# Optimization experiments

Measured on AMD Instinct MI355X. Metric: run time of the kernel, lower is better.

The kernel has to match this reference:

```python
import jax, jax.numpy as jnp
import numpy as np

B, S, D_MODEL = 4, 2048, 1024
H, DK, DV = 16, 64, 64
MASKED = False


def setup_inputs() -> dict:
    key = jax.random.key(0)
    ks = jax.random.split(key, 7)
    return {
        "q": jax.random.normal(ks[0], (B, S, D_MODEL), dtype=jnp.float32),
        "k": jax.random.normal(ks[1], (B, S, D_MODEL), dtype=jnp.float32),
        "v": jax.random.normal(ks[2], (B, S, D_MODEL), dtype=jnp.float32),
        "Wq": jax.random.normal(ks[3], (H, D_MODEL, DK), dtype=jnp.float32) * 0.05,
        "Wk": jax.random.normal(ks[4], (H, D_MODEL, DK), dtype=jnp.float32) * 0.05,
        "Wv": jax.random.normal(ks[5], (H, D_MODEL, DV), dtype=jnp.float32) * 0.05,
        "Wo": jax.random.normal(ks[6], (H * DV, D_MODEL), dtype=jnp.float32) * 0.05,
    }


def reference(q, k, v, Wq, Wk, Wv, Wo):
    # Per-head projections, batched over heads instead of a Python loop.
    Q = jnp.einsum("bsd,hdk->bhsk", q, Wq)  # [B,H,S,Dk]
    K = jnp.einsum("btd,hdk->bhtk", k, Wk)  # [B,H,S,Dk]
    V = jnp.einsum("btd,hdv->bhtv", v, Wv)  # [B,H,S,Dv]

    scale = 1.0 / jnp.sqrt(jnp.asarray(DK, dtype=Q.dtype))
    scores = jnp.einsum("bhsk,bhtk->bhst", Q, K) * scale  # [B,H,S,S]
    if MASKED:
        causal = jnp.tril(jnp.ones((S, S), dtype=bool))
        scores = jnp.where(causal, scores, jnp.finfo(scores.dtype).min)
    attn = jax.nn.softmax(scores, axis=-1)
    heads = jnp.einsum("bhst,bhtv->bhsv", attn, V)  # [B,H,S,Dv]

    # concat heads along feature dim (tf.concat(heads, axis=-1)) then Wo projection
    multi = heads.transpose(0, 2, 1, 3).reshape(q.shape[0], q.shape[1], H * DV)
    return multi @ Wo  # [B,S,D_MODEL]
```

## Files before the change

### kernel.cpp

```cpp
#include <hip/hip_runtime.h>
#include <hip/hip_bf16.h>

typedef __attribute__((ext_vector_type(8))) short short8;
typedef __attribute__((ext_vector_type(4))) short short4v;
typedef __attribute__((ext_vector_type(4))) float f32x4;
typedef __attribute__((ext_vector_type(2))) float f32x2;
typedef __attribute__((ext_vector_type(4))) unsigned short us4;
typedef __attribute__((ext_vector_type(2))) unsigned int u32x2;

#define NB 4
#define SEQ 2048
#define DMODEL 1024
#define NH 16
#define DHEAD 64
#define QSCALE 0.18033688011112042f
#define FM 34.0f

static __device__ __forceinline__ unsigned short f2bf(float f) {
    __hip_bfloat16 h = __float2bfloat16(f);
    return *reinterpret_cast<unsigned short*>(&h);
}
static __device__ __forceinline__ unsigned int cvt_pk(float lo, float hi) {
    float2 t; t.x = lo; t.y = hi;
    __hip_bfloat162 h = __float22bfloat162_rn(t);
    return *reinterpret_cast<unsigned int*>(&h);
}

typedef __attribute__((address_space(3))) unsigned int lds_u32_t;
typedef __attribute__((address_space(1))) const unsigned int glob_u32_t;
static __device__ __forceinline__ void gl_lds16(const unsigned short* g, unsigned short* l) {
    __builtin_amdgcn_global_load_lds((glob_u32_t*)g, (lds_u32_t*)l, 16, 0, 0);
}

__global__ __launch_bounds__(256) void prep_all(const float* __restrict__ q,
                                                const float* __restrict__ k,
                                                const float* __restrict__ v,
                                                const float* __restrict__ wq,
                                                const float* __restrict__ wk,
                                                const float* __restrict__ wv,
                                                const float* __restrict__ wo,
                                                unsigned short* __restrict__ xq,
                                                unsigned short* __restrict__ xk,
                                                unsigned short* __restrict__ xv,
                                                unsigned short* __restrict__ oq,
                                                unsigned short* __restrict__ ok,
                                                unsigned short* __restrict__ ov,
                                                unsigned short* __restrict__ oo) {
    const int z = blockIdx.y;
    int i = blockIdx.x * 256 + threadIdx.x;
    if (z < 3) {
        const float* in = z == 0 ? q : (z == 1 ? k : v);
        unsigned short* out = z == 0 ? xq : (z == 1 ? xk : xv);
        f32x4 val = ((const f32x4*)in)[i];
        u32x2 o;
        o.x = cvt_pk(val.x, val.y);
        o.y = cvt_pk(val.z, val.w);
        ((u32x2*)out)[i] = o;
    } else {
        if (i >= NH * DMODEL * DHEAD) return;
        if (z < 6) {
            const float* w = z == 3 ? wq : (z == 4 ? wk : wv);
            unsigned short* out = z == 3 ? oq : (z == 4 ? ok : ov);
            float scale = z == 3 ? QSCALE : 1.0f;
            int kk = i & 63;
            int d  = (i >> 6) & 1023;
            int h  = i >> 16;
            out[(size_t)(h * 64 + kk) * DMODEL + d] = f2bf(w[i] * scale);
        } else {
            int c = i & 1023;
            int r = i >> 10;
            oo[(size_t)c * 1024 + r] = f2bf(wo[i]);
        }
    }
}

struct GemmAcc { f32x4 a[4][4]; };

static __device__ __forceinline__ void gemm_core(const unsigned short* __restrict__ A,
                                                 const unsigned short* __restrict__ Bt,
                                                 unsigned short (*As)[4096],
                                                 unsigned short (*Bs)[4096],
                                                 int m0, int n0, int K, GemmAcc& acc) {
    const int tid = threadIdx.x;
    const int w = tid >> 6, l = tid & 63;
    const int lane16 = l & 15, quad = l >> 4;
    const int wr = w >> 1, wc = w & 1;

#pragma unroll
    for (int a = 0; a < 4; a++)
#pragma unroll
        for (int b = 0; b < 4; b++) acc.a[a][b] = (f32x4){0.f, 0.f, 0.f, 0.f};

    const int i0 = 2 * w, i1 = 2 * w + 1;
    const int rs = l >> 2;
    const int cc = ((l & 3) ^ ((l >> 3) & 3)) * 8;
    const unsigned short* a0 = A + (size_t)(m0 + i0 * 16 + rs) * K + cc;
    const unsigned short* a1 = A + (size_t)(m0 + i1 * 16 + rs) * K + cc;
    const unsigned short* b0 = Bt + (size_t)(n0 + i0 * 16 + rs) * K + cc;
    const unsigned short* b1 = Bt + (size_t)(n0 + i1 * 16 + rs) * K + cc;

    const int cl = (quad ^ ((lane16 >> 1) & 3)) * 8;
    const int ra = (wr * 64 + lane16) * 32 + cl;
    const int rb = (wc * 64 + lane16) * 32 + cl;

    for (int k0 = 0; k0 < K; k0 += 64) {
        __syncthreads();
#pragma unroll
        for (int h = 0; h < 2; h++) {
            gl_lds16(a0 + k0 + h * 32, &As[h][i0 * 512]);
            gl_lds16(a1 + k0 + h * 32, &As[h][i1 * 512]);
            gl_lds16(b0 + k0 + h * 32, &Bs[h][i0 * 512]);
            gl_lds16(b1 + k0 + h * 32, &Bs[h][i1 * 512]);
        }
        __syncthreads();
#pragma unroll
        for (int h = 0; h < 2; h++) {
            short8 af[4], bf[4];
#pragma unroll
            for (int mt = 0; mt < 4; mt++) af[mt] = *(const short8*)&As[h][ra + mt * 512];
#pragma unroll
            for (int nt = 0; nt < 4; nt++) bf[nt] = *(const short8*)&Bs[h][rb + nt * 512];
#pragma unroll
            for (int mt = 0; mt < 4; mt++)
#pragma unroll
                for (int nt = 0; nt < 4; nt++)
                    acc.a[mt][nt] = __builtin_amdgcn_mfma_f32_16x16x32_bf16(
                        af[mt], bf[nt], acc.a[mt][nt], 0, 0, 0);
        }
    }
}

__global__ __launch_bounds__(256) void gemm_qkv(const unsigned short* __restrict__ xq,
                                                const unsigned short* __restrict__ xk,
                                                const unsigned short* __restrict__ xv,
                                                const unsigned short* __restrict__ wq,
                                                const unsigned short* __restrict__ wk,
                                                const unsigned short* __restrict__ wv,
                                                unsigned short* __restrict__ Qb,
                                                unsigned short* __restrict__ Kb,
                                                unsigned short* __restrict__ Vtb) {
    __shared__ unsigned short As[2][4096];
    __shared__ unsigned short Bs[2][4096];
    const int z = blockIdx.z;
    const unsigned short* A = z == 0 ? xq : (z == 1 ? xk : xv);
    const unsigned short* Bt = z == 0 ? wq : (z == 1 ? wk : wv);
    unsigned short* out = z == 0 ? Qb : (z == 1 ? Kb : Vtb);

    const int m0 = blockIdx.x * 128, n0 = blockIdx.y * 128;
    GemmAcc acc;
    gemm_core(A, Bt, As, Bs, m0, n0, DMODEL, acc);

    const int l = threadIdx.x & 63, w = threadIdx.x >> 6;
    const int lane16 = l & 15, quad = l >> 4;
    const int wr = w >> 1, wc = w & 1;
    if (z < 2) {
#pragma unroll
        for (int mt = 0; mt < 4; mt++)
#pragma unroll
            for (int nt = 0; nt < 4; nt++)
#pragma unroll
                for (int r = 0; r < 4; r++) {
                    int m = m0 + wr * 64 + mt * 16 + quad * 4 + r;
                    int n = n0 + wc * 64 + nt * 16 + lane16;
                    int b_ = m >> 11, s = m & 2047, h = n >> 6, kk = n & 63;
                    out[((size_t)((b_ * NH + h) * SEQ + s) << 6) + kk] = f2bf(acc.a[mt][nt][r]);
                }
    } else {
#pragma unroll
        for (int mt = 0; mt < 4; mt++)
#pragma unroll
            for (int nt = 0; nt < 4; nt++) {
                int m = m0 + wr * 64 + mt * 16 + quad * 4;
                int n = n0 + wc * 64 + nt * 16 + lane16;
                int b_ = m >> 11, s = m & 2047, h = n >> 6, kk = n & 63;
                u32x2 pk;
                pk.x = cvt_pk(acc.a[mt][nt][0], acc.a[mt][nt][1]);
                pk.y = cvt_pk(acc.a[mt][nt][2], acc.a[mt][nt][3]);
                *(u32x2*)&out[(size_t)((b_ * NH + h) * DHEAD + kk) * SEQ + s] = pk;
            }
    }
}

__global__ __launch_bounds__(256) void gemm_out(const unsigned short* __restrict__ A,
                                                const unsigned short* __restrict__ Bt,
                                                float* __restrict__ C) {
    __shared__ unsigned short As[2][4096];
    __shared__ unsigned short Bs[2][4096];
    const int m0 = blockIdx.x * 128, n0 = blockIdx.y * 128;
    GemmAcc acc;
    gemm_core(A, Bt, As, Bs, m0, n0, DMODEL, acc);

    const int l = threadIdx.x & 63, w = threadIdx.x >> 6;
    const int lane16 = l & 15, quad = l >> 4;
    const int wr = w >> 1, wc = w & 1;
#pragma unroll
    for (int mt = 0; mt < 4; mt++)
#pragma unroll
        for (int nt = 0; nt < 4; nt++)
#pragma unroll
            for (int r = 0; r < 4; r++) {
                int m = m0 + wr * 64 + mt * 16 + quad * 4 + r;
                int n = n0 + wc * 64 + nt * 16 + lane16;
                C[(size_t)m * DMODEL + n] = acc.a[mt][nt][r];
            }
}

__global__ __launch_bounds__(256) void flash_attn(const unsigned short* __restrict__ Q,
                                                  const unsigned short* __restrict__ Kg,
                                                  const unsigned short* __restrict__ Vt,
                                                  unsigned short* __restrict__ Hout) {
    __shared__ unsigned short Ks[64 * 64];
    __shared__ unsigned short Vs[64 * 64];

    const int tid = threadIdx.x;
    const int w = tid >> 6, l = tid & 63;
    const int lane16 = l & 15, quad = l >> 4;
    const int bh = blockIdx.x & 63, b_ = bh >> 4, h = bh & 15;
    const int s0 = (blockIdx.x >> 6) * 128;

    const unsigned short* Qbh = Q + (size_t)bh * SEQ * DHEAD;
    const unsigned short* Kbh = Kg + (size_t)bh * SEQ * DHEAD;
    const unsigned short* Vbh = Vt + (size_t)bh * DHEAD * SEQ;

    short8 qf[2][2];
#pragma unroll
    for (int qm = 0; qm < 2; qm++)
#pragma unroll
        for (int ks = 0; ks < 2; ks++)
            qf[qm][ks] = *(const short8*)(Qbh +
                (size_t)(s0 + w * 32 + qm * 16 + lane16) * DHEAD + ks * 32 + quad * 8);

    f32x4 o[2][4];
#pragma unroll
    for (int qm = 0; qm < 2; qm++)
#pragma unroll
        for (int dt = 0; dt < 4; dt++) o[qm][dt] = (f32x4){0.f, 0.f, 0.f, 0.f};
    f32x2 lsum2[2];
    lsum2[0] = (f32x2){0.f, 0.f};
    lsum2[1] = (f32x2){0.f, 0.f};
    const f32x4 scinit = (f32x4){-FM, -FM, -FM, -FM};

    const int i0 = 2 * w, i1 = 2 * w + 1;
    const int rs = l >> 3;
    const int cgs = ((l & 7) ^ rs) * 8;
    const unsigned short* kg0 = Kbh + (size_t)(i0 * 8 + rs) * DHEAD + cgs;
    const unsigned short* kg1 = Kbh + (size_t)(i1 * 8 + rs) * DHEAD + cgs;
    const unsigned short* vg0 = Vbh + (size_t)(i0 * 8 + rs) * SEQ + cgs;
    const unsigned short* vg1 = Vbh + (size_t)(i1 * 8 + rs) * SEQ + cgs;
    unsigned short* lk0 = &Ks[i0 * 512];
    unsigned short* lk1 = &Ks[i1 * 512];
    unsigned short* lv0 = &Vs[i0 * 512];
    unsigned short* lv1 = &Vs[i1 * 512];

    const int swz = lane16 & 7;

    for (int t0 = 0; t0 < SEQ; t0 += 64) {
        __syncthreads();
        gl_lds16(kg0 + (size_t)t0 * DHEAD, lk0);
        gl_lds16(kg1 + (size_t)t0 * DHEAD, lk1);
        gl_lds16(vg0 + t0, lv0);
        gl_lds16(vg1 + t0, lv1);
        __syncthreads();

        short4v pf[2][4];
#pragma unroll
        for (int nt = 0; nt < 4; nt++) {
            const int kbase = (nt * 16 + lane16) * 64;
            short8 kf0 = *(const short8*)&Ks[kbase + ((quad ^ swz) * 8)];
            short8 kf1 = *(const short8*)&Ks[kbase + (((4 + quad) ^ swz) * 8)];
#pragma unroll
            for (int qm = 0; qm < 2; qm++) {
                f32x4 sc = __builtin_amdgcn_mfma_f32_16x16x32_bf16(kf0, qf[qm][0], scinit, 0, 0, 0);
                sc = __builtin_amdgcn_mfma_f32_16x16x32_bf16(kf1, qf[qm][1], sc, 0, 0, 0);
                float p0 = __builtin_amdgcn_exp2f(sc.x);
                float p1 = __builtin_amdgcn_exp2f(sc.y);
                float p2 = __builtin_amdgcn_exp2f(sc.z);
                float p3 = __builtin_amdgcn_exp2f(sc.w);
                f32x2 pa; pa.x = p0; pa.y = p1;
                f32x2 pb; pb.x = p2; pb.y = p3;
                lsum2[qm] += pa;
                lsum2[qm] += pb;
                u32x2 pk;
                pk.x = cvt_pk(p0, p1);
                pk.y = cvt_pk(p2, p3);
                pf[qm][nt] = __builtin_bit_cast(short4v, pk);
            }
        }
#pragma unroll
        for (int nt = 0; nt < 4; nt++) {
#pragma unroll
            for (int dt = 0; dt < 4; dt++) {
                int cl = (2 * nt + (quad >> 1)) ^ swz;
                short4v vf = *(const short4v*)&Vs[(dt * 16 + lane16) * 64 + cl * 8 + (quad & 1) * 4];
                o[0][dt] = __builtin_amdgcn_mfma_f32_16x16x16bf16_1k(vf, pf[0][nt], o[0][dt], 0, 0, 0);
                o[1][dt] = __builtin_amdgcn_mfma_f32_16x16x16bf16_1k(vf, pf[1][nt], o[1][dt], 0, 0, 0);
            }
        }
    }

    float lsum[2];
#pragma unroll
    for (int qm = 0; qm < 2; qm++) {
        float s = lsum2[qm].x + lsum2[qm].y;
        s += __shfl_xor(s, 16);
        s += __shfl_xor(s, 32);
        lsum[qm] = s;
    }
#pragma unroll
    for (int qm = 0; qm < 2; qm++) {
        float inv = 1.f / lsum[qm];
        int s = s0 + w * 32 + qm * 16 + lane16;
        size_t rowbase = (size_t)(b_ * SEQ + s) * DMODEL + h * 64;
#pragma unroll
        for (int dt = 0; dt < 4; dt++) {
            u32x2 ov;
            ov.x = cvt_pk(o[qm][dt][0] * inv, o[qm][dt][1] * inv);
            ov.y = cvt_pk(o[qm][dt][2] * inv, o[qm][dt][3] * inv);
            *(u32x2*)&Hout[rowbase + dt * 16 + quad * 4] = ov;
        }
    }
}

extern "C" void kernel_launch(void* const* d_in, const int* in_sizes, int n_in,
                              void* d_out, int out_size, void* d_ws, size_t ws_size,
                              hipStream_t stream) {
    const float* q  = (const float*)d_in[0];
    const float* k  = (const float*)d_in[1];
    const float* v  = (const float*)d_in[2];
    const float* Wq = (const float*)d_in[3];
    const float* Wk = (const float*)d_in[4];
    const float* Wv = (const float*)d_in[5];
    const float* Wo = (const float*)d_in[6];

    const size_t SZ_X = (size_t)NB * SEQ * DMODEL * 2;
    const size_t SZ_W = (size_t)DMODEL * DMODEL * 2;
    char* ws = (char*)d_ws;
    unsigned short* xq  = (unsigned short*)(ws);
    unsigned short* xk  = (unsigned short*)(ws + SZ_X);
    unsigned short* xv  = (unsigned short*)(ws + 2 * SZ_X);
    unsigned short* wqt = (unsigned short*)(ws + 3 * SZ_X);
    unsigned short* wkt = (unsigned short*)(ws + 3 * SZ_X + SZ_W);
    unsigned short* wvt = (unsigned short*)(ws + 3 * SZ_X + 2 * SZ_W);
    unsigned short* wot = (unsigned short*)(ws + 3 * SZ_X + 3 * SZ_W);
    unsigned short* Qb  = (unsigned short*)(ws + 3 * SZ_X + 4 * SZ_W);
    unsigned short* Kb  = (unsigned short*)(ws + 4 * SZ_X + 4 * SZ_W);
    unsigned short* Vtb = (unsigned short*)(ws + 5 * SZ_X + 4 * SZ_W);
    unsigned short* hd  = (unsigned short*)(ws + 6 * SZ_X + 4 * SZ_W);
    if (ws_size < 7 * SZ_X + 4 * SZ_W) return;

    const int n4 = NB * SEQ * DMODEL / 4;
    prep_all<<<dim3(n4 / 256, 7), 256, 0, stream>>>(q, k, v, Wq, Wk, Wv, Wo,
                                                    xq, xk, xv, wqt, wkt, wvt, wot);

    const int M = NB * SEQ;
    gemm_qkv<<<dim3(M / 128, DMODEL / 128, 3), 256, 0, stream>>>(
        xq, xk, xv, wqt, wkt, wvt, Qb, Kb, Vtb);

    flash_attn<<<dim3((SEQ / 128) * NB * NH), 256, 0, stream>>>(Qb, Kb, Vtb, hd);

    gemm_out<<<dim3(M / 128, DMODEL / 128), 256, 0, stream>>>(hd, wot, (float*)d_out);
}
```

Baseline: 358.6 us.

## Switch flash attention to 32x32 MFMA tiles with permuted V layout

```diff
diff --git a/kernel.cpp b/kernel.cpp
--- a/kernel.cpp
+++ b/kernel.cpp
@@ -5,6 +5,7 @@
 typedef __attribute__((ext_vector_type(4))) short short4v;
 typedef __attribute__((ext_vector_type(4))) float f32x4;
 typedef __attribute__((ext_vector_type(2))) float f32x2;
+typedef __attribute__((ext_vector_type(16))) float f32x16;
 typedef __attribute__((ext_vector_type(4))) unsigned short us4;
 typedef __attribute__((ext_vector_type(2))) unsigned int u32x2;
 
@@ -166,13 +167,15 @@
                     out[((size_t)((b_ * NH + h) * SEQ + s) << 6) + kk] = f2bf(acc.a[mt][nt][r]);
                 }
     } else {
+        const int sperm_off = ((quad & 1) << 3) | ((quad >> 1) << 2);
 #pragma unroll
         for (int mt = 0; mt < 4; mt++)
 #pragma unroll
             for (int nt = 0; nt < 4; nt++) {
-                int m = m0 + wr * 64 + mt * 16 + quad * 4;
+                int m = m0 + wr * 64 + mt * 16;
                 int n = n0 + wc * 64 + nt * 16 + lane16;
-                int b_ = m >> 11, s = m & 2047, h = n >> 6, kk = n & 63;
+                int b_ = m >> 11, s16 = m & 2047, h = n >> 6, kk = n & 63;
+                int s = s16 + sperm_off;
                 u32x2 pk;
                 pk.x = cvt_pk(acc.a[mt][nt][0], acc.a[mt][nt][1]);
                 pk.y = cvt_pk(acc.a[mt][nt][2], acc.a[mt][nt][3]);
@@ -214,7 +217,7 @@
 
     const int tid = threadIdx.x;
     const int w = tid >> 6, l = tid & 63;
-    const int lane16 = l & 15, quad = l >> 4;
+    const int l32 = l & 31, hi = l >> 5;
     const int bh = blockIdx.x & 63, b_ = bh >> 4, h = bh & 15;
     const int s0 = (blockIdx.x >> 6) * 128;
 
@@ -222,23 +225,21 @@
     const unsigned short* Kbh = Kg + (size_t)bh * SEQ * DHEAD;
     const unsigned short* Vbh = Vt + (size_t)bh * DHEAD * SEQ;
 
-    short8 qf[2][2];
-#pragma unroll
-    for (int qm = 0; qm < 2; qm++)
-#pragma unroll
-        for (int ks = 0; ks < 2; ks++)
-            qf[qm][ks] = *(const short8*)(Qbh +
-                (size_t)(s0 + w * 32 + qm * 16 + lane16) * DHEAD + ks * 32 + quad * 8);
-
-    f32x4 o[2][4];
-#pragma unroll
-    for (int qm = 0; qm < 2; qm++)
-#pragma unroll
-        for (int dt = 0; dt < 4; dt++) o[qm][dt] = (f32x4){0.f, 0.f, 0.f, 0.f};
-    f32x2 lsum2[2];
-    lsum2[0] = (f32x2){0.f, 0.f};
-    lsum2[1] = (f32x2){0.f, 0.f};
-    const f32x4 scinit = (f32x4){-FM, -FM, -FM, -FM};
+    short8 qf[4];
+#pragma unroll
+    for (int kb = 0; kb < 4; kb++)
+        qf[kb] = *(const short8*)(Qbh +
+            (size_t)(s0 + w * 32 + l32) * DHEAD + kb * 16 + hi * 8);
+
+    f32x16 o[2];
+#pragma unroll
+    for (int dt = 0; dt < 2; dt++)
+#pragma unroll
+        for (int r = 0; r < 16; r++) o[dt][r] = 0.f;
+    f32x2 lsum2 = (f32x2){0.f, 0.f};
+    f32x16 scinit;
+#pragma unroll
+    for (int r = 0; r < 16; r++) scinit[r] = -FM;
 
     const int i0 = 2 * w, i1 = 2 * w + 1;
     const int rs = l >> 3;
@@ -252,7 +253,7 @@
     unsigned short* lv0 = &Vs[i0 * 512];
     unsigned short* lv1 = &Vs[i1 * 512];
 
-    const int swz = lane16 & 7;
+    const int swz = l & 7;
 
     for (int t0 = 0; t0 < SEQ; t0 += 64) {
         __syncthreads();
@@ -262,61 +263,61 @@
         gl_lds16(vg1 + t0, lv1);
         __syncthreads();
 
-        short4v pf[2][4];
-#pragma unroll
-        for (int nt = 0; nt < 4; nt++) {
-            const int kbase = (nt * 16 + lane16) * 64;
-            short8 kf0 = *(const short8*)&Ks[kbase + ((quad ^ swz) * 8)];
-            short8 kf1 = *(const short8*)&Ks[kbase + (((4 + quad) ^ swz) * 8)];
-#pragma unroll
-            for (int qm = 0; qm < 2; qm++) {
-                f32x4 sc = __builtin_amdgcn_mfma_f32_16x16x32_bf16(kf0, qf[qm][0], scinit, 0, 0, 0);
-                sc = __builtin_amdgcn_mfma_f32_16x16x32_bf16(kf1, qf[qm][1], sc, 0, 0, 0);
-                float p0 = __builtin_amdgcn_exp2f(sc.x);
-                float p1 = __builtin_amdgcn_exp2f(sc.y);
-                float p2 = __builtin_amdgcn_exp2f(sc.z);
-                float p3 = __builtin_amdgcn_exp2f(sc.w);
+        short4v pf[8];
+#pragma unroll
+        for (int rb = 0; rb < 2; rb++) {
+            f32x16 sc = scinit;
+#pragma unroll
+            for (int kb = 0; kb < 4; kb++) {
+                short8 kf = *(const short8*)&Ks[(rb * 32 + l32) * 64 +
+                                                 (((2 * kb + hi) ^ swz) * 8)];
+                sc = __builtin_amdgcn_mfma_f32_32x32x16_bf16(kf, qf[kb], sc, 0, 0, 0);
+            }
+#pragma unroll
+            for (int rq = 0; rq < 4; rq++) {
+                float p0 = __builtin_amdgcn_exp2f(sc[4 * rq + 0]);
+                float p1 = __builtin_amdgcn_exp2f(sc[4 * rq + 1]);
+                float p2 = __builtin_amdgcn_exp2f(sc[4 * rq + 2]);
+                float p3 = __builtin_amdgcn_exp2f(sc[4 * rq + 3]);
                 f32x2 pa; pa.x = p0; pa.y = p1;
                 f32x2 pb; pb.x = p2; pb.y = p3;
-                lsum2[qm] += pa;
-                lsum2[qm] += pb;
+                lsum2 += pa;
+                lsum2 += pb;
                 u32x2 pk;
                 pk.x = cvt_pk(p0, p1);
                 pk.y = cvt_pk(p2, p3);
-                pf[qm][nt] = __builtin_bit_cast(short4v, pk);
-            }
-        }
-#pragma unroll
-        for (int nt = 0; nt < 4; nt++) {
-#pragma unroll
-            for (int dt = 0; dt < 4; dt++) {
-                int cl = (2 * nt + (quad >> 1)) ^ swz;
-                short4v vf = *(const short4v*)&Vs[(dt * 16 + lane16) * 64 + cl * 8 + (quad & 1) * 4];
-                o[0][dt] = __builtin_amdgcn_mfma_f32_16x16x16bf16_1k(vf, pf[0][nt], o[0][dt], 0, 0, 0);
-                o[1][dt] = __builtin_amdgcn_mfma_f32_16x16x16bf16_1k(vf, pf[1][nt], o[1][dt], 0, 0, 0);
-            }
-        }
-    }
-
-    float lsum[2];
-#pragma unroll
-    for (int qm = 0; qm < 2; qm++) {
-        float s = lsum2[qm].x + lsum2[qm].y;
-        s += __shfl_xor(s, 16);
-        s += __shfl_xor(s, 32);
-        lsum[qm] = s;
-    }
-#pragma unroll
-    for (int qm = 0; qm < 2; qm++) {
-        float inv = 1.f / lsum[qm];
-        int s = s0 + w * 32 + qm * 16 + lane16;
-        size_t rowbase = (size_t)(b_ * SEQ + s) * DMODEL + h * 64;
-#pragma unroll
-        for (int dt = 0; dt < 4; dt++) {
+                pf[rb * 4 + rq] = __builtin_bit_cast(short4v, pk);
+            }
+        }
+
+#pragma unroll
+        for (int dt = 0; dt < 2; dt++) {
+#pragma unroll
+            for (int a2 = 0; a2 < 4; a2++) {
+                short8 vv = *(const short8*)&Vs[(dt * 32 + l32) * 64 +
+                                                 (((2 * a2 + hi) ^ swz) * 8)];
+                short4v vlo = __builtin_shufflevector(vv, vv, 0, 1, 2, 3);
+                short4v vhi = __builtin_shufflevector(vv, vv, 4, 5, 6, 7);
+                o[dt] = __builtin_amdgcn_mfma_f32_32x32x8bf16_1k(vlo, pf[2 * a2], o[dt], 0, 0, 0);
+                o[dt] = __builtin_amdgcn_mfma_f32_32x32x8bf16_1k(vhi, pf[2 * a2 + 1], o[dt], 0, 0, 0);
+            }
+        }
+    }
+
+    float lsum = lsum2.x + lsum2.y;
+    lsum += __shfl_xor(lsum, 32);
+    const float inv = 1.f / lsum;
+
+    const int sq = s0 + w * 32 + l32;
+    const size_t rowbase = (size_t)(b_ * SEQ + sq) * DMODEL + h * 64;
+#pragma unroll
+    for (int dt = 0; dt < 2; dt++) {
+#pragma unroll
+        for (int rq = 0; rq < 4; rq++) {
             u32x2 ov;
-            ov.x = cvt_pk(o[qm][dt][0] * inv, o[qm][dt][1] * inv);
-            ov.y = cvt_pk(o[qm][dt][2] * inv, o[qm][dt][3] * inv);
-            *(u32x2*)&Hout[rowbase + dt * 16 + quad * 4] = ov;
+            ov.x = cvt_pk(o[dt][4 * rq + 0] * inv, o[dt][4 * rq + 1] * inv);
+            ov.y = cvt_pk(o[dt][4 * rq + 2] * inv, o[dt][4 * rq + 3] * inv);
+            *(u32x2*)&Hout[rowbase + dt * 32 + rq * 8 + hi * 4] = ov;
         }
     }
 }
```

Result: no change. 361.1 us (+0.7%).
